# Performance work log

Measured on AMD Instinct MI355X. Metric: run time of the kernel, lower is better.

The kernel has to match this reference:

```python
import jax, jax.numpy as jnp
import numpy as np


def setup_inputs() -> dict:
    key = jax.random.key(0)
    kx, kq, kb, kc = jax.random.split(key, 4)
    N, D = 16384, 1024
    x = jax.random.normal(kx, (N, D), dtype=jnp.float32)
    Q = jax.random.normal(kq, (D, D), dtype=jnp.float32)
    b = jax.random.normal(kb, (D,), dtype=jnp.float32)
    c = jax.random.normal(kc, (1,), dtype=jnp.float32)
    return {"x": x, "Q": Q, "b": b, "c": c}


def reference(x, Q, b, c):
    # y_i = x_i^T Q x_i + b^T x_i + c  (same math as diag(x @ Q @ x.T)
    # without materializing the NxN matrix)
    xQ = x @ Q                                # [N, D]
    quad = jnp.sum(xQ * x, axis=-1)           # [N]
    y = quad + x @ b + c                       # [N] (c broadcasts from [1])
    return y[:, None]                          # [N, 1]
```

## Files before the change

kernel.cpp:

```cpp
#include <hip/hip_runtime.h>
#include <hip/hip_bf16.h>


#define DD 1024
#define TROWB 2048
#define XROW 264

typedef short v8s __attribute__((ext_vector_type(8)));
typedef float v4f __attribute__((ext_vector_type(4)));

__device__ __forceinline__ short f2b(float f) {
    union { __hip_bfloat16 h; short s; } u;
    u.h = __float2bfloat16(f);
    return u.s;
}
__device__ __forceinline__ float b2f(short s) {
    union { unsigned u; float f; } uu;
    uu.u = ((unsigned)(unsigned short)s) << 16;
    return uu.f;
}

__global__ __launch_bounds__(512, 2)
void quad_kernel(const float* __restrict__ x, const float* __restrict__ Q,
                 const float* __restrict__ bvec, const float* __restrict__ cptr,
                 float* __restrict__ y)
{
    __shared__ __align__(16) char  tile[2][16 * TROWB];
    __shared__ __align__(16) short xvb[2][64 * XROW];
    __shared__ float yred[4][64];

    const int tid  = threadIdx.x;
    const int lane = tid & 63;
    const int wave = tid >> 6;
    const int quad = lane >> 4;
    const int l15  = lane & 15;
    const int kq   = wave & 3;
    const int rg   = wave >> 2;

    const int row_base = blockIdx.x * 64;

    float4 pf[8];
    #pragma unroll
    for (int i = 0; i < 8; ++i) {
        const int idx = tid + i * 512;
        pf[i] = *(const float4*)(Q + (size_t)(idx >> 8) * DD + (idx & 255) * 4);
    }

    v8s a[2][8];
    #pragma unroll
    for (int g = 0; g < 2; ++g) {
        const float* xr = x + (size_t)(row_base + rg * 32 + g * 16 + l15) * DD + kq * 256 + quad * 8;
        #pragma unroll
        for (int s = 0; s < 8; ++s) {
            const float4 f0 = *(const float4*)(xr + s * 32);
            const float4 f1 = *(const float4*)(xr + s * 32 + 4);
            v8s t;
            t[0]=f2b(f0.x); t[1]=f2b(f0.y); t[2]=f2b(f0.z); t[3]=f2b(f0.w);
            t[4]=f2b(f1.x); t[5]=f2b(f1.y); t[6]=f2b(f1.z); t[7]=f2b(f1.w);
            a[g][s] = t;
            asm volatile("" : "+a"(a[g][s]));
        }
    }

    if (kq == 0) {
        #pragma unroll
        for (int g = 0; g < 2; ++g) {
            char* d = (char*)&xvb[0][(size_t)(rg * 32 + g * 16 + l15) * XROW];
            #pragma unroll
            for (int s = 0; s < 8; ++s)
                *(v8s*)(d + s * 64 + quad * 16) = a[g][s];
        }
    }

    #pragma unroll
    for (int i = 0; i < 8; ++i) {
        const int idx = tid + i * 512;
        const int row = idx >> 8, slot = idx & 255;
        const float4 f = pf[i];
        short4 s4; s4.x=f2b(f.x); s4.y=f2b(f.y); s4.z=f2b(f.z); s4.w=f2b(f.w);
        *(short4*)(&tile[0][row * TROWB + ((slot * 8) ^ ((row & 7) << 4))]) = s4;
    }
    #pragma unroll
    for (int i = 0; i < 8; ++i) {
        const int idx = tid + i * 512;
        pf[i] = *(const float4*)(Q + (size_t)(16 + (idx >> 8)) * DD + (idx & 255) * 4);
    }
    __syncthreads();

    const int xorc = (l15 & 7) << 4;
    float acc[2][4];
    #pragma unroll
    for (int g = 0; g < 2; ++g)
        #pragma unroll
        for (int r = 0; r < 4; ++r) acc[g][r] = 0.f;

    for (int t = 0; t < 64; ++t) {
        if (t < 63) {
            char* db = &tile[(t + 1) & 1][0];
            #pragma unroll
            for (int i = 0; i < 8; ++i) {
                const int idx = tid + i * 512;
                const int row = idx >> 8, slot = idx & 255;
                const float4 f = pf[i];
                short4 s4; s4.x=f2b(f.x); s4.y=f2b(f.y); s4.z=f2b(f.z); s4.w=f2b(f.w);
                *(short4*)(db + row * TROWB + ((slot * 8) ^ ((row & 7) << 4))) = s4;
            }
            if (t < 62) {
                #pragma unroll
                for (int i = 0; i < 8; ++i) {
                    const int idx = tid + i * 512;
                    pf[i] = *(const float4*)(Q + (size_t)((t + 2) * 16 + (idx >> 8)) * DD + (idx & 255) * 4);
                }
            }
        }

        if ((t & 15) == 0 && t < 48 && kq == (t >> 4) + 1) {
            const int nb = ((t >> 4) + 1) & 1;
            #pragma unroll
            for (int g = 0; g < 2; ++g) {
                char* d = (char*)&xvb[nb][(size_t)(rg * 32 + g * 16 + l15) * XROW];
                #pragma unroll
                for (int s = 0; s < 8; ++s)
                    *(v8s*)(d + s * 64 + quad * 16) = a[g][s];
            }
        }

        const float bb = (kq == 0) ? bvec[t * 16 + l15] : 0.f;

        const char* tb = &tile[t & 1][0] + l15 * TROWB;
        v4f cf[2];
        cf[0] = (v4f){0.f, 0.f, 0.f, 0.f};
        cf[1] = (v4f){0.f, 0.f, 0.f, 0.f};
        #pragma unroll
        for (int s = 0; s < 8; ++s) {
            const v8s bf = *(const v8s*)(tb + ((kq * 512 + s * 64 + quad * 16) ^ xorc));
            cf[0] = __builtin_amdgcn_mfma_f32_16x16x32_bf16(a[0][s], bf, cf[0], 0, 0, 0);
            cf[1] = __builtin_amdgcn_mfma_f32_16x16x32_bf16(a[1][s], bf, cf[1], 0, 0, 0);
        }

        const short* xp = &xvb[(t >> 4) & 1][0] + (t & 15) * 16 + l15;
        #pragma unroll
        for (int g = 0; g < 2; ++g)
            #pragma unroll
            for (int r = 0; r < 4; ++r) {
                const int row = rg * 32 + g * 16 + quad * 4 + r;
                acc[g][r] += (cf[g][r] + bb) * b2f(xp[(size_t)row * XROW]);
            }

        __syncthreads();
    }

    #pragma unroll
    for (int g = 0; g < 2; ++g)
        #pragma unroll
        for (int r = 0; r < 4; ++r) {
            float v = acc[g][r];
            v += __shfl_xor(v, 1); v += __shfl_xor(v, 2);
            v += __shfl_xor(v, 4); v += __shfl_xor(v, 8);
            if (l15 == 0)
                yred[kq][rg * 32 + g * 16 + quad * 4 + r] = v;
        }
    __syncthreads();
    if (tid < 64)
        y[row_base + tid] = yred[0][tid] + yred[1][tid] + yred[2][tid] + yred[3][tid] + cptr[0];
}

extern "C" void kernel_launch(void* const* d_in, const int* in_sizes, int n_in,
                              void* d_out, int out_size, void* d_ws, size_t ws_size,
                              hipStream_t stream)
{
    const float* x = (const float*)d_in[0];
    const float* Q = (const float*)d_in[1];
    const float* b = (const float*)d_in[2];
    const float* c = (const float*)d_in[3];
    float* y = (float*)d_out;

    quad_kernel<<<dim3(256), dim3(512), 0, stream>>>(x, Q, b, c, y);
}
```

Baseline: 167.6 us.

## Pre-convert Q to swizzled bf16 tiles and stream them via direct global-to-LDS loads

Adds a separate kernel that converts Q to bf16 once, in the swizzled tile layout, and stores it in the workspace. The main kernel then copies each tile straight into LDS with global_load_lds on a triple buffer, replacing the per-block fp32 loads, conversions and LDS stores. It also halves the x staging buffer granularity and swaps __syncthreads for explicit waitcnt plus a barrier. The aim is to cut the duplicated fp32 Q traffic and conversion work across all 256 blocks, at the cost of an extra kernel launch and trickier hand-written synchronisation.

```diff
diff --git a/kernel.cpp b/kernel.cpp
--- a/kernel.cpp
+++ b/kernel.cpp
@@ -3,8 +3,9 @@
 
 
 #define DD 1024
-#define TROWB 2048
-#define XROW 264
+#define TILEB 32768
+#define XROWS 136
+#define XPH (64 * XROWS)
 
 typedef short v8s __attribute__((ext_vector_type(8)));
 typedef float v4f __attribute__((ext_vector_type(4)));
@@ -20,13 +21,31 @@
     return uu.f;
 }
 
+#define MFMA16(A, B, C) __builtin_amdgcn_mfma_f32_16x16x32_bf16(A, B, C, 0, 0, 0)
+
+__global__ __launch_bounds__(256, 4)
+void cvt_kernel(const float* __restrict__ Q, char* __restrict__ qb)
+{
+    const int gid = blockIdx.x * 256 + threadIdx.x;
+    const int n  = gid >> 7;
+    const int k0 = (gid & 127) * 8;
+    const float4 f0 = *(const float4*)(Q + (size_t)n * DD + k0);
+    const float4 f1 = *(const float4*)(Q + (size_t)n * DD + k0 + 4);
+    v8s t;
+    t[0]=f2b(f0.x); t[1]=f2b(f0.y); t[2]=f2b(f0.z); t[3]=f2b(f0.w);
+    t[4]=f2b(f1.x); t[5]=f2b(f1.y); t[6]=f2b(f1.z); t[7]=f2b(f1.w);
+    char* dst = qb + (size_t)(n >> 4) * TILEB + (size_t)(n & 15) * 2048
+              + (((unsigned)(k0 * 2)) ^ (((unsigned)n & 7u) << 4));
+    *(v8s*)dst = t;
+}
+
 __global__ __launch_bounds__(512, 2)
-void quad_kernel(const float* __restrict__ x, const float* __restrict__ Q,
+void quad_kernel(const float* __restrict__ x, const char* __restrict__ qb,
                  const float* __restrict__ bvec, const float* __restrict__ cptr,
                  float* __restrict__ y)
 {
-    __shared__ __align__(16) char  tile[2][16 * TROWB];
-    __shared__ __align__(16) short xvb[2][64 * XROW];
+    __shared__ __align__(1024) char tile[3][TILEB];
+    __shared__ __align__(16) short xvb[2][XPH];
     __shared__ float yred[4][64];
 
     const int tid  = threadIdx.x;
@@ -38,18 +57,27 @@
     const int rg   = wave >> 2;
 
     const int row_base = blockIdx.x * 64;
-
-    float4 pf[8];
-    #pragma unroll
-    for (int i = 0; i < 8; ++i) {
-        const int idx = tid + i * 512;
-        pf[i] = *(const float4*)(Q + (size_t)(idx >> 8) * DD + (idx & 255) * 4);
-    }
+    const int xorc = (l15 & 7) << 4;
+
+    auto stage = [&](int buf, int t) {
+        const char* gp = qb + (size_t)t * TILEB + tid * 16;
+        char* lp = &tile[buf][0] + tid * 16;
+        #pragma unroll
+        for (int i = 0; i < 4; ++i)
+            __builtin_amdgcn_global_load_lds(
+                (const __attribute__((address_space(1))) unsigned int*)(gp + i * 8192),
+                (__attribute__((address_space(3))) unsigned int*)(lp + i * 8192),
+                16, 0, 0);
+    };
+
+    stage(0, 0);
+    stage(1, 1);
 
     v8s a[2][8];
     #pragma unroll
     for (int g = 0; g < 2; ++g) {
-        const float* xr = x + (size_t)(row_base + rg * 32 + g * 16 + l15) * DD + kq * 256 + quad * 8;
+        const float* xr = x + (size_t)(row_base + rg * 32 + g * 16 + l15) * DD
+                        + kq * 256 + quad * 8;
         #pragma unroll
         for (int s = 0; s < 8; ++s) {
             const float4 f0 = *(const float4*)(xr + s * 32);
@@ -65,29 +93,19 @@
     if (kq == 0) {
         #pragma unroll
         for (int g = 0; g < 2; ++g) {
-            char* d = (char*)&xvb[0][(size_t)(rg * 32 + g * 16 + l15) * XROW];
-            #pragma unroll
-            for (int s = 0; s < 8; ++s)
-                *(v8s*)(d + s * 64 + quad * 16) = a[g][s];
+            short* d = &xvb[0][(rg * 32 + g * 16 + l15) * XROWS + quad * 8];
+            *(v8s*)(d +  0) = a[g][0];
+            *(v8s*)(d + 32) = a[g][1];
+            *(v8s*)(d + 64) = a[g][2];
+            *(v8s*)(d + 96) = a[g][3];
         }
     }
 
-    #pragma unroll
-    for (int i = 0; i < 8; ++i) {
-        const int idx = tid + i * 512;
-        const int row = idx >> 8, slot = idx & 255;
-        const float4 f = pf[i];
-        short4 s4; s4.x=f2b(f.x); s4.y=f2b(f.y); s4.z=f2b(f.z); s4.w=f2b(f.w);
-        *(short4*)(&tile[0][row * TROWB + ((slot * 8) ^ ((row & 7) << 4))]) = s4;
-    }
-    #pragma unroll
-    for (int i = 0; i < 8; ++i) {
-        const int idx = tid + i * 512;
-        pf[i] = *(const float4*)(Q + (size_t)(16 + (idx >> 8)) * DD + (idx & 255) * 4);
-    }
-    __syncthreads();
-
-    const int xorc = (l15 & 7) << 4;
+    asm volatile("s_waitcnt lgkmcnt(0)" ::: "memory");
+    asm volatile("s_waitcnt vmcnt(4)" ::: "memory");
+    __builtin_amdgcn_s_barrier();
+    __builtin_amdgcn_sched_barrier(0);
+
     float acc[2][4];
     #pragma unroll
     for (int g = 0; g < 2; ++g)
@@ -95,59 +113,60 @@
         for (int r = 0; r < 4; ++r) acc[g][r] = 0.f;
 
     for (int t = 0; t < 64; ++t) {
-        if (t < 63) {
-            char* db = &tile[(t + 1) & 1][0];
-            #pragma unroll
-            for (int i = 0; i < 8; ++i) {
-                const int idx = tid + i * 512;
-                const int row = idx >> 8, slot = idx & 255;
-                const float4 f = pf[i];
-                short4 s4; s4.x=f2b(f.x); s4.y=f2b(f.y); s4.z=f2b(f.z); s4.w=f2b(f.w);
-                *(short4*)(db + row * TROWB + ((slot * 8) ^ ((row & 7) << 4))) = s4;
-            }
-            if (t < 62) {
-                #pragma unroll
-                for (int i = 0; i < 8; ++i) {
-                    const int idx = tid + i * 512;
-                    pf[i] = *(const float4*)(Q + (size_t)((t + 2) * 16 + (idx >> 8)) * DD + (idx & 255) * 4);
+        if (t + 2 < 64) stage((t + 2) % 3, t + 2);
+
+        if ((t & 7) == 0 && t < 56) {
+            const int ph = (t >> 3) + 1;
+            if (kq == (ph >> 1)) {
+                short* base = &xvb[ph & 1][0];
+                if (ph & 1) {
+                    #pragma unroll
+                    for (int g = 0; g < 2; ++g) {
+                        short* d = base + (rg * 32 + g * 16 + l15) * XROWS + quad * 8;
+                        *(v8s*)(d +  0) = a[g][4];
+                        *(v8s*)(d + 32) = a[g][5];
+                        *(v8s*)(d + 64) = a[g][6];
+                        *(v8s*)(d + 96) = a[g][7];
+                    }
+                } else {
+                    #pragma unroll
+                    for (int g = 0; g < 2; ++g) {
+                        short* d = base + (rg * 32 + g * 16 + l15) * XROWS + quad * 8;
+                        *(v8s*)(d +  0) = a[g][0];
+                        *(v8s*)(d + 32) = a[g][1];
+                        *(v8s*)(d + 64) = a[g][2];
+                        *(v8s*)(d + 96) = a[g][3];
+                    }
                 }
             }
         }
 
-        if ((t & 15) == 0 && t < 48 && kq == (t >> 4) + 1) {
-            const int nb = ((t >> 4) + 1) & 1;
-            #pragma unroll
-            for (int g = 0; g < 2; ++g) {
-                char* d = (char*)&xvb[nb][(size_t)(rg * 32 + g * 16 + l15) * XROW];
-                #pragma unroll
-                for (int s = 0; s < 8; ++s)
-                    *(v8s*)(d + s * 64 + quad * 16) = a[g][s];
-            }
-        }
-
         const float bb = (kq == 0) ? bvec[t * 16 + l15] : 0.f;
 
-        const char* tb = &tile[t & 1][0] + l15 * TROWB;
+        const char* tb = &tile[t % 3][0] + l15 * 2048;
         v4f cf[2];
         cf[0] = (v4f){0.f, 0.f, 0.f, 0.f};
         cf[1] = (v4f){0.f, 0.f, 0.f, 0.f};
         #pragma unroll
         for (int s = 0; s < 8; ++s) {
-            const v8s bf = *(const v8s*)(tb + ((kq * 512 + s * 64 + quad * 16) ^ xorc));
-            cf[0] = __builtin_amdgcn_mfma_f32_16x16x32_bf16(a[0][s], bf, cf[0], 0, 0, 0);
-            cf[1] = __builtin_amdgcn_mfma_f32_16x16x32_bf16(a[1][s], bf, cf[1], 0, 0, 0);
-        }
-
-        const short* xp = &xvb[(t >> 4) & 1][0] + (t & 15) * 16 + l15;
+            const v8s bf = *(const v8s*)(tb + (((unsigned)(kq * 512 + s * 64 + quad * 16)) ^ (unsigned)xorc));
+            cf[0] = MFMA16(a[0][s], bf, cf[0]);
+            cf[1] = MFMA16(a[1][s], bf, cf[1]);
+        }
+
+        const short* xp = &xvb[(t >> 3) & 1][0]
+                        + (rg * 32 + quad * 4) * XROWS + (t & 7) * 16 + l15;
         #pragma unroll
         for (int g = 0; g < 2; ++g)
             #pragma unroll
-            for (int r = 0; r < 4; ++r) {
-                const int row = rg * 32 + g * 16 + quad * 4 + r;
-                acc[g][r] += (cf[g][r] + bb) * b2f(xp[(size_t)row * XROW]);
-            }
-
-        __syncthreads();
+            for (int r = 0; r < 4; ++r)
+                acc[g][r] += (cf[g][r] + bb) * b2f(xp[(g * 16 + r) * XROWS]);
+
+        asm volatile("s_waitcnt lgkmcnt(0)" ::: "memory");
+        if (t + 2 < 64) asm volatile("s_waitcnt vmcnt(4)" ::: "memory");
+        else            asm volatile("s_waitcnt vmcnt(0)" ::: "memory");
+        __builtin_amdgcn_s_barrier();
+        __builtin_amdgcn_sched_barrier(0);
     }
 
     #pragma unroll
@@ -162,7 +181,8 @@
         }
     __syncthreads();
     if (tid < 64)
-        y[row_base + tid] = yred[0][tid] + yred[1][tid] + yred[2][tid] + yred[3][tid] + cptr[0];
+        y[row_base + tid] = yred[0][tid] + yred[1][tid] + yred[2][tid]
+                          + yred[3][tid] + cptr[0];
 }
 
 extern "C" void kernel_launch(void* const* d_in, const int* in_sizes, int n_in,
@@ -174,6 +194,8 @@
     const float* b = (const float*)d_in[2];
     const float* c = (const float*)d_in[3];
     float* y = (float*)d_out;
-
-    quad_kernel<<<dim3(256), dim3(512), 0, stream>>>(x, Q, b, c, y);
-}
+    char* qb = (char*)d_ws;
+
+    cvt_kernel<<<dim3(512), dim3(256), 0, stream>>>(Q, qb);
+    quad_kernel<<<dim3(256), dim3(512), 0, stream>>>(x, qb, b, c, y);
+}
```

New measurement: 160.2 us. -4.4%, faster.
